# Kernel tuning notes

Measured on AMD Instinct MI355X. Metric: run time of the kernel, lower is better.

Reference implementation:

```python
import jax, jax.numpy as jnp
import numpy as np

B, T, H, LAT, ADIM = 8192, 40, 100, 10, 2
ATT_TEMP = 5.0


def setup_inputs() -> dict:
    key = jax.random.key(0)
    ks = jax.random.split(key, 12)
    return {
        "sampled_att_z": jax.random.normal(ks[0], (B, LAT), jnp.float32),
        "enc_h": jax.random.normal(ks[1], (B, H), jnp.float32),
        # keep IDM params strictly positive / physically plausible to avoid inf
        "idm_params": 1.0 + 2.0 * jax.random.uniform(ks[2], (B, 5), jnp.float32),
        "idm_s": jax.random.uniform(ks[3], (B, T, 8), jnp.float32),
        "sdv_acts": jax.random.normal(ks[4], (B, T, ADIM), jnp.float32),
        "linear_W": jax.random.normal(ks[5], (LAT, H), jnp.float32) / np.float32(np.sqrt(LAT)),
        "linear_b": jnp.zeros((H,), jnp.float32),
        "lstm_Wx": jax.random.normal(ks[6], (H + ADIM, 4 * H), jnp.float32) / np.float32(np.sqrt(H + ADIM)),
        "lstm_Wh": jax.random.normal(ks[7], (H, 4 * H), jnp.float32) / np.float32(np.sqrt(H)),
        "lstm_b": jnp.zeros((4 * H,), jnp.float32),
        "att_W": jax.random.normal(ks[8], (H, 1), jnp.float32) / np.float32(np.sqrt(H)),
        "att_b": jnp.zeros((1,), jnp.float32),
        # precomputed per-step noise, replacing tf.random.normal inside the loop
        "noise_f": jax.random.normal(ks[9], (T, B, 1), jnp.float32),
        "noise_m": jax.random.normal(ks[10], (T, B, 1), jnp.float32),
    }


def reference(sampled_att_z, enc_h, idm_params, idm_s, sdv_acts,
              linear_W, linear_b, lstm_Wx, lstm_Wh, lstm_b, att_W, att_b,
              noise_f, noise_m):
    desired_v = idm_params[:, 0:1]
    desired_tgap = idm_params[:, 1:2]
    min_jamx = idm_params[:, 2:3]
    max_act = idm_params[:, 3:4]
    min_act = idm_params[:, 4:5]

    def idm_driver(vel, dv, dx):  # all [B,1]
        dx = jnp.clip(dx, 0.5, 1000.0)
        desired_gap = min_jamx + jax.nn.relu(
            desired_tgap * vel + vel * dv / (2.0 * jnp.sqrt(max_act * min_act)))
        act = max_act * (1.0 - (vel / desired_v) ** 4 - (desired_gap / dx) ** 2)
        return jnp.clip(act, -3.0, 3.0)

    att_proj = sampled_att_z @ linear_W + linear_b  # [B,H]; also the att_context and init h,c

    s_tm = jnp.swapaxes(idm_s, 0, 1)      # [T,B,8]
    a_tm = jnp.swapaxes(sdv_acts, 0, 1)   # [T,B,ADIM]

    ego_v0 = idm_s[:, 0, 0:1]
    ego_x0 = idm_s[:, 0, 3:4]
    zero_act = jnp.zeros_like(ego_v0)  # step-0 kinematic update is a no-op

    def step(carry, xs):
        ego_v, ego_x, h, c, act = carry
        s, sdv, nf, nm = xs
        ego_v = ego_v + act * 0.1
        ego_x = ego_x + ego_v * 0.1 + 0.5 * act * 0.1 ** 2

        f_v, m_v = s[:, 1:2], s[:, 2:3]
        f_x, m_x = s[:, 4:5], s[:, 5:6]
        f_ex, m_ex = s[:, 6:7], s[:, 7:8]

        ef_act = idm_driver(ego_v, ego_v - f_v, f_x - ego_x)
        ef_act = f_ex * ef_act + (1.0 - f_ex) * nf
        em_act = idm_driver(ego_v, ego_v - m_v, m_x - ego_x)
        em_act = m_ex * em_act + (1.0 - m_ex) * nm

        x_in = jnp.concatenate([att_proj, sdv], axis=-1)  # [B,H+ADIM]
        z = x_in @ lstm_Wx + h @ lstm_Wh + lstm_b          # [B,4H], keras gate order i,f,g,o
        zi, zf, zg, zo = jnp.split(z, 4, axis=-1)
        c = jax.nn.sigmoid(zf) * c + jax.nn.sigmoid(zi) * jnp.tanh(zg)
        h = jax.nn.sigmoid(zo) * jnp.tanh(c)

        att_score = jax.nn.sigmoid(ATT_TEMP * (h @ att_W + att_b))  # [B,1]
        act = (1.0 - att_score) * ef_act + att_score * em_act
        return (ego_v, ego_x, h, c, act), (act, att_score)

    init = (ego_v0, ego_x0, att_proj, att_proj, zero_act)
    _, (acts, atts) = jax.lax.scan(step, init, (s_tm, a_tm, noise_f, noise_m))
    act_seq = jnp.swapaxes(acts, 0, 1)  # [B,T,1]
    att_seq = jnp.swapaxes(atts, 0, 1)  # [B,T,1]
    return act_seq, att_seq
```

## Files before the change

### kernel.cpp

```cpp
#include <hip/hip_runtime.h>
#include <math.h>


#define B_TOT 8192
#define T_STEPS 40
#define NB 16

typedef _Float16 f16;
typedef f16 f16x8 __attribute__((ext_vector_type(8)));
typedef float f32x4 __attribute__((ext_vector_type(4)));

__device__ __forceinline__ float rcpf(float x) { return __builtin_amdgcn_rcpf(x); }
__device__ __forceinline__ float ex2(float x)  { return __builtin_amdgcn_exp2f(x); }
__device__ __forceinline__ float sigf(float x)  { return rcpf(1.f + ex2(-1.44269504f * x)); }


__global__ __launch_bounds__(256) void idm_prep(
    const float* __restrict__ Wx, const float* __restrict__ Wh,
    const float* __restrict__ bvec, const float* __restrict__ attw,
    const float* __restrict__ attB,
    f16* __restrict__ whb, f16* __restrict__ wxb,
    float* __restrict__ bp)
{
  int i = blockIdx.x * 256 + threadIdx.x;
  int k = i >> 9, n = i & 511;
  int g = n >> 7, j128 = n & 127;
  float sc = (g == 2) ? 2.88539008f : 1.44269504f;
  float vh = 0.f, vx = 0.f;
  if (j128 < 100) {
    int col = g * 100 + j128;
    if (k < 100)      { vh = Wh[k * 400 + col] * sc; vx = Wx[k * 400 + col] * sc; }
    else if (k < 102) { vh = Wx[k * 400 + col] * sc; }
  } else if (n == 100 && k < 100) {
    vh = attw[k];
  }
  int idx = (((n >> 4) * 4 + (k >> 5)) * 64 + (((k >> 3) & 3) * 16 + (n & 15))) * 8 + (k & 7);
  whb[idx] = (f16)vh;
  wxb[idx] = (f16)vx;
  if (i < 512) {
    int gg = i >> 7, jj = i & 127;
    float scb = (gg == 2) ? 2.88539008f : 1.44269504f;
    bp[i] = (jj < 100) ? bvec[gg * 100 + jj] * scb
                       : ((i == 100) ? attB[0] : 0.f);
  }
}

#define MM(z, a, g, kf) z = __builtin_amdgcn_mfma_f32_16x16x32_f16(a, wb[g][kf], z, 0, 0, 0)

#define TAIL_STEP(tt) {                                                        \
    int tt_ = (tt);                                                            \
    float inv_dv = pS[0][l], des_tg = pS[1][l], min_jx = pS[2][l];             \
    float max_a = pS[3][l], inv2s = pS[4][l];                                  \
    float2 s01 = *(const float2*)&sS[l][tt_][0];                               \
    float2 s23 = *(const float2*)&sS[l][tt_][2];                               \
    float2 s45 = *(const float2*)&sS[l][tt_][4];                               \
    float nf = nS[0][tt_][l], nm = nS[1][tt_][l];                              \
    float lg = logitS[tt_][l];                                                 \
    ego_v += actT * 0.1f;                                                      \
    ego_x += ego_v * 0.1f + actT * 0.005f;                                     \
    float dxf = fminf(fmaxf(s23.x - ego_x, 0.5f), 1000.f);                     \
    float dgf = min_jx + fmaxf(0.f, des_tg * ego_v + ego_v * (ego_v - s01.x) * inv2s); \
    float rr = ego_v * inv_dv; float rr2 = rr * rr;                            \
    float qf = dgf * rcpf(dxf);                                                \
    float af_ = fminf(fmaxf(max_a * (1.f - rr2 * rr2 - qf * qf), -3.f), 3.f);  \
    float dxm = fminf(fmaxf(s23.y - ego_x, 0.5f), 1000.f);                     \
    float dgm = min_jx + fmaxf(0.f, des_tg * ego_v + ego_v * (ego_v - s01.y) * inv2s); \
    float qm = dgm * rcpf(dxm);                                                \
    float am_ = fminf(fmaxf(max_a * (1.f - rr2 * rr2 - qm * qm), -3.f), 3.f);  \
    float ef2 = s45.x * af_ + (1.f - s45.x) * nf;                              \
    float em2 = s45.y * am_ + (1.f - s45.y) * nm;                              \
    float att = sigf(5.f * lg);                                                \
    actT = (1.f - att) * ef2 + att * em2;                                      \
    accS[0][l][tt_] = actT;                                                    \
    accS[1][l][tt_] = att;                                                     \
  }

__global__ __launch_bounds__(448, 4) void idm_main(
    const float* __restrict__ z_att,
    const float* __restrict__ linear_W,
    const float* __restrict__ linear_b,
    const float* __restrict__ sdv_acts,
    const f16* __restrict__ whb, const f16* __restrict__ wxb,
    const float* __restrict__ bp,
    const float* __restrict__ idm_params,
    const float* __restrict__ idm_s,
    const float* __restrict__ noise_f,
    const float* __restrict__ noise_m,
    float* __restrict__ out)
{
  __shared__ f16   hS[2][16][136];
  __shared__ f16   sdvS[T_STEPS][16][2];
  __shared__ float logitS[T_STEPS][16];
  __shared__ float sS[16][T_STEPS][6];
  __shared__ float nS[2][T_STEPS][16];
  __shared__ float accS[2][16][T_STEPS];
  __shared__ float pS[5][16];

  const int tid = threadIdx.x;
  const int w  = tid >> 6;
  const int l  = tid & 63;
  const int lr = l & 15;
  const int lq = l >> 4;
  const int b0g = blockIdx.x * NB;
  const int jcol = 16 * w + lr;
  const bool tail_lane = (tid < NB);

  for (int idx = tid; idx < 2176; idx += 448) ((unsigned*)hS)[idx] = 0u;
  for (int idx = tid; idx < 1280; idx += 448) {
    float v = sdv_acts[(size_t)b0g * 80 + idx];
    int b = idx / 80, r = idx - b * 80;
    sdvS[r >> 1][b][r & 1] = (f16)v;
  }
  for (int idx = tid; idx < 5120; idx += 448) {
    int f = idx & 7;
    if (f != 0 && f != 3) {
      int b = idx / 320, rem = idx - b * 320, t = rem >> 3;
      sS[b][t][(f < 3) ? f - 1 : f - 2] = idm_s[(size_t)b0g * 320 + idx];
    }
  }
  for (int idx = tid; idx < 1280; idx += 448) {
    int which = idx >= 640 ? 1 : 0;
    int r = idx - which * 640;
    int t = r >> 4, i = r & 15;
    nS[which][t][i] = which ? noise_m[(size_t)t * B_TOT + b0g + i]
                            : noise_f[(size_t)t * B_TOT + b0g + i];
  }
  if (tid < 80) pS[tid % 5][tid / 5] = idm_params[(size_t)b0g * 5 + tid];
  __syncthreads();

  if (tid < 16) {
    pS[0][tid] = rcpf(pS[0][tid]);
    pS[4][tid] = 0.5f / sqrtf(pS[3][tid] * pS[4][tid]);
  }

  if (tid >= 64 && tid < 320) {
    int s2 = tid - 64;
    int b = s2 >> 4, oct = s2 & 15;
    float za[10];
    #pragma unroll
    for (int t2 = 0; t2 < 10; ++t2) za[t2] = z_att[(b0g + b) * 10 + t2];
    #pragma unroll
    for (int jj = 0; jj < 8; ++jj) {
      int j = oct * 8 + jj;
      if (j < 100) {
        float acc = linear_b[j];
        #pragma unroll
        for (int t2 = 0; t2 < 10; ++t2) acc = fmaf(za[t2], linear_W[t2 * 100 + j], acc);
        hS[0][b][j] = (f16)acc;
      }
    }
  }
  if (tid < 32) hS[0][tid >> 1][100 + (tid & 1)] = sdvS[0][tid >> 1][tid & 1];
  __syncthreads();

  f16x8 wb[4][4];
  #pragma unroll
  for (int g = 0; g < 4; ++g) {
    int tile = w + 8 * g;
    #pragma unroll
    for (int kf = 0; kf < 4; ++kf)
      wb[g][kf] = *(const f16x8*)(wxb + ((size_t)(tile * 4 + kf) * 64 + l) * 8);
  }
  f32x4 cx[4];
  #pragma unroll
  for (int g = 0; g < 4; ++g) {
    float bpv = bp[(w + 8 * g) * 16 + lr];
    f32x4 c = {bpv, bpv, bpv, bpv};
    cx[g] = c;
  }
  #pragma unroll
  for (int kf = 0; kf < 4; ++kf) {
    f16x8 a = *(const f16x8*)(&hS[0][lr][kf * 32 + lq * 8]);
    #pragma unroll
    for (int g = 0; g < 4; ++g)
      cx[g] = __builtin_amdgcn_mfma_f32_16x16x32_f16(a, wb[g][kf], cx[g], 0, 0, 0);
  }
  #pragma unroll
  for (int g = 0; g < 4; ++g) {
    int tile = w + 8 * g;
    #pragma unroll
    for (int kf = 0; kf < 4; ++kf)
      wb[g][kf] = *(const f16x8*)(whb + ((size_t)(tile * 4 + kf) * 64 + l) * 8);
  }

  float cst[4];
  #pragma unroll
  for (int r = 0; r < 4; ++r) cst[r] = (float)hS[0][lq * 4 + r][jcol];

  float ego_v = 0.f, ego_x = 0.f, actT = 0.f;
  if (tail_lane) {
    ego_v = idm_s[(size_t)(b0g + l) * 320 + 0];
    ego_x = idm_s[(size_t)(b0g + l) * 320 + 3];
  }

  int p = 0;
  for (int t = 0; t < T_STEPS; ++t) {
    f16x8 a0 = *(const f16x8*)(&hS[p][lr][0  + lq * 8]);
    f16x8 a1 = *(const f16x8*)(&hS[p][lr][32 + lq * 8]);
    f16x8 a2 = *(const f16x8*)(&hS[p][lr][64 + lq * 8]);
    f16x8 a3 = *(const f16x8*)(&hS[p][lr][96 + lq * 8]);
    f32x4 z0 = cx[0], z1 = cx[1], z2 = cx[2], z3 = cx[3];
    MM(z0,a0,0,0); MM(z1,a0,1,0); MM(z2,a0,2,0); MM(z3,a0,3,0);
    MM(z0,a1,0,1); MM(z1,a1,1,1); MM(z2,a1,2,1); MM(z3,a1,3,1);
    MM(z0,a2,0,2); MM(z1,a2,1,2); MM(z2,a2,2,2); MM(z3,a2,3,2);
    MM(z0,a3,0,3); MM(z1,a3,1,3); MM(z2,a3,2,3); MM(z3,a3,3,3);

    if (w == 6 && t > 0 && lr == 4) {
      #pragma unroll
      for (int r = 0; r < 4; ++r) logitS[t - 1][lq * 4 + r] = z0[r];
    }

    #pragma unroll
    for (int r = 0; r < 4; ++r) {
      float e0 = ex2(-z0[r]);
      float e1 = ex2(-z1[r]);
      float e2 = fminf(ex2(z2[r]), 1e30f);
      float e3 = ex2(-z3[r]);
      float sf  = rcpf(1.f + e1);
      float itg = (e2 - 1.f) * rcpf((1.f + e0) * (1.f + e2));
      float cc  = fmaf(sf, cst[r], itg);
      float d   = fminf(ex2(2.88539008f * cc), 1e30f);
      float hh  = (d - 1.f) * rcpf((1.f + e3) * (1.f + d));
      cst[r] = cc;
      if (jcol < 100) hS[p ^ 1][lq * 4 + r][jcol] = (f16)hh;
    }
    if (t + 1 < T_STEPS && tid < 32)
      hS[p ^ 1][tid >> 1][100 + (tid & 1)] = sdvS[t + 1][tid >> 1][tid & 1];
    if (tail_lane && t >= 2) TAIL_STEP(t - 2);
    __syncthreads();
    p ^= 1;
  }

  if (w == 6) {
    float bpv6 = bp[96 + lr];
    f32x4 zL = {bpv6, bpv6, bpv6, bpv6};
    #pragma unroll
    for (int kf = 0; kf < 4; ++kf) {
      f16x8 a = *(const f16x8*)(&hS[p][lr][kf * 32 + lq * 8]);
      zL = __builtin_amdgcn_mfma_f32_16x16x32_f16(a, wb[0][kf], zL, 0, 0, 0);
    }
    if (lr == 4) {
      #pragma unroll
      for (int r = 0; r < 4; ++r) logitS[T_STEPS - 1][lq * 4 + r] = zL[r];
    }
  }
  if (tail_lane) TAIL_STEP(T_STEPS - 2);
  __syncthreads();
  if (tail_lane) TAIL_STEP(T_STEPS - 1);
  __syncthreads();

  if (tid < 160) {
    f32x4 va = ((const f32x4*)&accS[0][0][0])[tid];
    f32x4 vt = ((const f32x4*)&accS[1][0][0])[tid];
    *(f32x4*)(out + (size_t)b0g * T_STEPS + tid * 4) = va;
    *(f32x4*)(out + (size_t)B_TOT * T_STEPS + (size_t)b0g * T_STEPS + tid * 4) = vt;
  }
}

extern "C" void kernel_launch(void* const* d_in, const int* in_sizes, int n_in,
                              void* d_out, int out_size, void* d_ws, size_t ws_size,
                              hipStream_t stream) {
  const float* z_att      = (const float*)d_in[0];
  const float* idm_params = (const float*)d_in[2];
  const float* idm_s      = (const float*)d_in[3];
  const float* sdv_acts   = (const float*)d_in[4];
  const float* linear_W   = (const float*)d_in[5];
  const float* linear_b   = (const float*)d_in[6];
  const float* lstm_Wx    = (const float*)d_in[7];
  const float* lstm_Wh    = (const float*)d_in[8];
  const float* lstm_b     = (const float*)d_in[9];
  const float* att_W      = (const float*)d_in[10];
  const float* att_b      = (const float*)d_in[11];
  const float* noise_f    = (const float*)d_in[12];
  const float* noise_m    = (const float*)d_in[13];
  float* out = (float*)d_out;

  f16*   whb = (f16*)d_ws;
  f16*   wxb = (f16*)((char*)d_ws + 131072);
  float* bp  = (float*)((char*)d_ws + 262144);

  idm_prep<<<256, 256, 0, stream>>>(lstm_Wx, lstm_Wh, lstm_b, att_W, att_b,
                                    whb, wxb, bp);
  idm_main<<<B_TOT / NB, 448, 0, stream>>>(z_att, linear_W, linear_b, sdv_acts,
                                           whb, wxb, bp,
                                           idm_params, idm_s,
                                           noise_f, noise_m, out);
}
```

Baseline: 174.8 us.

## Ping-pong two batch groups per block to overlap MFMA with gate math

Doubles the batch rows per block to 32 and splits the 14 waves into two groups of 16 rows each. The groups alternate each half-step, so one group's MFMA gate matmul runs while the other group does the transcendental LSTM cell update and IDM tail. The aim is to hide the serial dependency between the matmul and the elementwise work within one block. The cost is twice as many block barriers per timestep and half as many blocks, which may cut the natural overlap the hardware already gets from co-resident blocks.

```diff
diff --git a/kernel.cpp b/kernel.cpp
--- a/kernel.cpp
+++ b/kernel.cpp
@@ -4,7 +4,7 @@
 
 #define B_TOT 8192
 #define T_STEPS 40
-#define NB 16
+#define NB 32
 
 typedef _Float16 f16;
 typedef f16 f16x8 __attribute__((ext_vector_type(8)));
@@ -47,15 +47,15 @@
 
 #define MM(z, a, g, kf) z = __builtin_amdgcn_mfma_f32_16x16x32_f16(a, wb[g][kf], z, 0, 0, 0)
 
-#define TAIL_STEP(tt) {                                                        \
-    int tt_ = (tt);                                                            \
-    float inv_dv = pS[0][l], des_tg = pS[1][l], min_jx = pS[2][l];             \
-    float max_a = pS[3][l], inv2s = pS[4][l];                                  \
-    float2 s01 = *(const float2*)&sS[l][tt_][0];                               \
-    float2 s23 = *(const float2*)&sS[l][tt_][2];                               \
-    float2 s45 = *(const float2*)&sS[l][tt_][4];                               \
-    float nf = nS[0][tt_][l], nm = nS[1][tt_][l];                              \
-    float lg = logitS[tt_][l];                                                 \
+#define TAIL_STEP(tt, lb) {                                                    \
+    int tt_ = (tt); int lb_ = (lb);                                            \
+    float inv_dv = pS[0][lb_], des_tg = pS[1][lb_], min_jx = pS[2][lb_];       \
+    float max_a = pS[3][lb_], inv2s = pS[4][lb_];                              \
+    float2 s01 = *(const float2*)&sS[lb_][tt_][0];                             \
+    float2 s23 = *(const float2*)&sS[lb_][tt_][2];                             \
+    float2 s45 = *(const float2*)&sS[lb_][tt_][4];                             \
+    float nf = nS[0][tt_][lb_], nm = nS[1][tt_][lb_];                          \
+    float lg = logitS[tt_][lb_];                                               \
     ego_v += actT * 0.1f;                                                      \
     ego_x += ego_v * 0.1f + actT * 0.005f;                                     \
     float dxf = fminf(fmaxf(s23.x - ego_x, 0.5f), 1000.f);                     \
@@ -71,11 +71,11 @@
     float em2 = s45.y * am_ + (1.f - s45.y) * nm;                              \
     float att = sigf(5.f * lg);                                                \
     actT = (1.f - att) * ef2 + att * em2;                                      \
-    accS[0][l][tt_] = actT;                                                    \
-    accS[1][l][tt_] = att;                                                     \
-  }
-
-__global__ __launch_bounds__(448, 4) void idm_main(
+    accS[0][lb_][tt_] = actT;                                                  \
+    accS[1][lb_][tt_] = att;                                                   \
+  }
+
+__global__ __launch_bounds__(896, 4) void idm_main(
     const float* __restrict__ z_att,
     const float* __restrict__ linear_W,
     const float* __restrict__ linear_b,
@@ -89,56 +89,57 @@
     float* __restrict__ out)
 {
   __shared__ f16   hS[2][16][136];
-  __shared__ f16   sdvS[T_STEPS][16][2];
-  __shared__ float logitS[T_STEPS][16];
-  __shared__ float sS[16][T_STEPS][6];
-  __shared__ float nS[2][T_STEPS][16];
-  __shared__ float accS[2][16][T_STEPS];
-  __shared__ float pS[5][16];
+  __shared__ f16   sdvS[T_STEPS][32][2];
+  __shared__ float logitS[T_STEPS][32];
+  __shared__ float sS[32][T_STEPS][6];
+  __shared__ float nS[2][T_STEPS][32];
+  __shared__ float accS[2][32][T_STEPS];
+  __shared__ float pS[5][32];
 
   const int tid = threadIdx.x;
-  const int w  = tid >> 6;
+  const int w   = tid >> 6;
+  const int grp = (w >= 7) ? 1 : 0;
+  const int wv  = grp ? (w - 7) : w;
   const int l  = tid & 63;
   const int lr = l & 15;
   const int lq = l >> 4;
   const int b0g = blockIdx.x * NB;
-  const int jcol = 16 * w + lr;
-  const bool tail_lane = (tid < NB);
-
-  for (int idx = tid; idx < 2176; idx += 448) ((unsigned*)hS)[idx] = 0u;
-  for (int idx = tid; idx < 1280; idx += 448) {
+  const int jcol = 16 * wv + lr;
+
+  for (int idx = tid; idx < 2176; idx += 896) ((unsigned*)hS)[idx] = 0u;
+  for (int idx = tid; idx < 2560; idx += 896) {
     float v = sdv_acts[(size_t)b0g * 80 + idx];
     int b = idx / 80, r = idx - b * 80;
     sdvS[r >> 1][b][r & 1] = (f16)v;
   }
-  for (int idx = tid; idx < 5120; idx += 448) {
+  for (int idx = tid; idx < 10240; idx += 896) {
     int f = idx & 7;
     if (f != 0 && f != 3) {
       int b = idx / 320, rem = idx - b * 320, t = rem >> 3;
       sS[b][t][(f < 3) ? f - 1 : f - 2] = idm_s[(size_t)b0g * 320 + idx];
     }
   }
-  for (int idx = tid; idx < 1280; idx += 448) {
-    int which = idx >= 640 ? 1 : 0;
-    int r = idx - which * 640;
-    int t = r >> 4, i = r & 15;
+  for (int idx = tid; idx < 2560; idx += 896) {
+    int which = idx >= 1280 ? 1 : 0;
+    int r = idx - which * 1280;
+    int t = r >> 5, i = r & 31;
     nS[which][t][i] = which ? noise_m[(size_t)t * B_TOT + b0g + i]
                             : noise_f[(size_t)t * B_TOT + b0g + i];
   }
-  if (tid < 80) pS[tid % 5][tid / 5] = idm_params[(size_t)b0g * 5 + tid];
-  __syncthreads();
-
-  if (tid < 16) {
+  if (tid < 160) pS[tid % 5][tid / 5] = idm_params[(size_t)b0g * 5 + tid];
+  __syncthreads();
+
+  if (tid < 32) {
     pS[0][tid] = rcpf(pS[0][tid]);
     pS[4][tid] = 0.5f / sqrtf(pS[3][tid] * pS[4][tid]);
   }
 
-  if (tid >= 64 && tid < 320) {
+  if (tid >= 64 && tid < 576) {
     int s2 = tid - 64;
-    int b = s2 >> 4, oct = s2 & 15;
+    int lb = s2 >> 4, oct = s2 & 15;
     float za[10];
     #pragma unroll
-    for (int t2 = 0; t2 < 10; ++t2) za[t2] = z_att[(b0g + b) * 10 + t2];
+    for (int t2 = 0; t2 < 10; ++t2) za[t2] = z_att[(size_t)(b0g + lb) * 10 + t2];
     #pragma unroll
     for (int jj = 0; jj < 8; ++jj) {
       int j = oct * 8 + jj;
@@ -146,17 +147,17 @@
         float acc = linear_b[j];
         #pragma unroll
         for (int t2 = 0; t2 < 10; ++t2) acc = fmaf(za[t2], linear_W[t2 * 100 + j], acc);
-        hS[0][b][j] = (f16)acc;
-      }
-    }
-  }
-  if (tid < 32) hS[0][tid >> 1][100 + (tid & 1)] = sdvS[0][tid >> 1][tid & 1];
+        hS[lb >> 4][lb & 15][j] = (f16)acc;
+      }
+    }
+  }
+  if (tid < 64) hS[tid >> 5][(tid >> 1) & 15][100 + (tid & 1)] = sdvS[0][tid >> 1][tid & 1];
   __syncthreads();
 
   f16x8 wb[4][4];
   #pragma unroll
   for (int g = 0; g < 4; ++g) {
-    int tile = w + 8 * g;
+    int tile = wv + 8 * g;
     #pragma unroll
     for (int kf = 0; kf < 4; ++kf)
       wb[g][kf] = *(const f16x8*)(wxb + ((size_t)(tile * 4 + kf) * 64 + l) * 8);
@@ -164,20 +165,20 @@
   f32x4 cx[4];
   #pragma unroll
   for (int g = 0; g < 4; ++g) {
-    float bpv = bp[(w + 8 * g) * 16 + lr];
+    float bpv = bp[(wv + 8 * g) * 16 + lr];
     f32x4 c = {bpv, bpv, bpv, bpv};
     cx[g] = c;
   }
   #pragma unroll
   for (int kf = 0; kf < 4; ++kf) {
-    f16x8 a = *(const f16x8*)(&hS[0][lr][kf * 32 + lq * 8]);
+    f16x8 a = *(const f16x8*)(&hS[grp][lr][kf * 32 + lq * 8]);
     #pragma unroll
     for (int g = 0; g < 4; ++g)
       cx[g] = __builtin_amdgcn_mfma_f32_16x16x32_f16(a, wb[g][kf], cx[g], 0, 0, 0);
   }
   #pragma unroll
   for (int g = 0; g < 4; ++g) {
-    int tile = w + 8 * g;
+    int tile = wv + 8 * g;
     #pragma unroll
     for (int kf = 0; kf < 4; ++kf)
       wb[g][kf] = *(const f16x8*)(whb + ((size_t)(tile * 4 + kf) * 64 + l) * 8);
@@ -185,31 +186,73 @@
 
   float cst[4];
   #pragma unroll
-  for (int r = 0; r < 4; ++r) cst[r] = (float)hS[0][lq * 4 + r][jcol];
+  for (int r = 0; r < 4; ++r) cst[r] = (float)hS[grp][lq * 4 + r][jcol];
 
   float ego_v = 0.f, ego_x = 0.f, actT = 0.f;
-  if (tail_lane) {
-    ego_v = idm_s[(size_t)(b0g + l) * 320 + 0];
-    ego_x = idm_s[(size_t)(b0g + l) * 320 + 3];
-  }
-
-  int p = 0;
-  for (int t = 0; t < T_STEPS; ++t) {
-    f16x8 a0 = *(const f16x8*)(&hS[p][lr][0  + lq * 8]);
-    f16x8 a1 = *(const f16x8*)(&hS[p][lr][32 + lq * 8]);
-    f16x8 a2 = *(const f16x8*)(&hS[p][lr][64 + lq * 8]);
-    f16x8 a3 = *(const f16x8*)(&hS[p][lr][96 + lq * 8]);
-    f32x4 z0 = cx[0], z1 = cx[1], z2 = cx[2], z3 = cx[3];
-    MM(z0,a0,0,0); MM(z1,a0,1,0); MM(z2,a0,2,0); MM(z3,a0,3,0);
-    MM(z0,a1,0,1); MM(z1,a1,1,1); MM(z2,a1,2,1); MM(z3,a1,3,1);
-    MM(z0,a2,0,2); MM(z1,a2,1,2); MM(z2,a2,2,2); MM(z3,a2,3,2);
-    MM(z0,a3,0,3); MM(z1,a3,1,3); MM(z2,a3,2,3); MM(z3,a3,3,3);
-
-    if (w == 6 && t > 0 && lr == 4) {
+  if (wv == 0 && l < 16) {
+    int b = b0g + grp * 16 + l;
+    ego_v = idm_s[(size_t)b * 320 + 0];
+    ego_x = idm_s[(size_t)b * 320 + 3];
+  }
+
+  f32x4 z0, z1, z2, z3;
+
+  for (int hi = 0; hi < 2 * T_STEPS; ++hi) {
+    int ph = hi & 1, step = hi >> 1;
+    if (ph == grp) {
+      f16x8 a0 = *(const f16x8*)(&hS[grp][lr][0  + lq * 8]);
+      f16x8 a1 = *(const f16x8*)(&hS[grp][lr][32 + lq * 8]);
+      f16x8 a2 = *(const f16x8*)(&hS[grp][lr][64 + lq * 8]);
+      f16x8 a3 = *(const f16x8*)(&hS[grp][lr][96 + lq * 8]);
+      z0 = cx[0]; z1 = cx[1]; z2 = cx[2]; z3 = cx[3];
+      MM(z0,a0,0,0); MM(z1,a0,1,0); MM(z2,a0,2,0); MM(z3,a0,3,0);
+      MM(z0,a1,0,1); MM(z1,a1,1,1); MM(z2,a1,2,1); MM(z3,a1,3,1);
+      MM(z0,a2,0,2); MM(z1,a2,1,2); MM(z2,a2,2,2); MM(z3,a2,3,2);
+      MM(z0,a3,0,3); MM(z1,a3,1,3); MM(z2,a3,2,3); MM(z3,a3,3,3);
+      if (wv == 6 && step > 0 && lr == 4) {
+        #pragma unroll
+        for (int r = 0; r < 4; ++r) logitS[step - 1][grp * 16 + lq * 4 + r] = z0[r];
+      }
+    } else {
+      int gstep = step - grp;
+      if (gstep >= 0) {
+        #pragma unroll
+        for (int r = 0; r < 4; ++r) {
+          float e0 = ex2(-z0[r]);
+          float e1 = ex2(-z1[r]);
+          float e2 = fminf(ex2(z2[r]), 1e30f);
+          float e3 = ex2(-z3[r]);
+          float sf  = rcpf(1.f + e1);
+          float itg = (e2 - 1.f) * rcpf((1.f + e0) * (1.f + e2));
+          float cc  = fmaf(sf, cst[r], itg);
+          float d   = fminf(ex2(2.88539008f * cc), 1e30f);
+          float hh  = (d - 1.f) * rcpf((1.f + e3) * (1.f + d));
+          cst[r] = cc;
+          if (jcol < 100) hS[grp][lq * 4 + r][jcol] = (f16)hh;
+        }
+        if (wv == 1 && l < 32 && gstep + 1 < T_STEPS)
+          hS[grp][l >> 1][100 + (l & 1)] = sdvS[gstep + 1][grp * 16 + (l >> 1)][l & 1];
+        if (wv == 0 && l < 16 && gstep >= 1) TAIL_STEP(gstep - 1, grp * 16 + l);
+      }
+    }
+    __syncthreads();
+  }
+
+  if (grp == 0) {
+    if (wv == 6) {
+      float bpv6 = bp[96 + lr];
+      f32x4 zL = {bpv6, bpv6, bpv6, bpv6};
       #pragma unroll
-      for (int r = 0; r < 4; ++r) logitS[t - 1][lq * 4 + r] = z0[r];
-    }
-
+      for (int kf = 0; kf < 4; ++kf) {
+        f16x8 a = *(const f16x8*)(&hS[0][lr][kf * 32 + lq * 8]);
+        zL = __builtin_amdgcn_mfma_f32_16x16x32_f16(a, wb[0][kf], zL, 0, 0, 0);
+      }
+      if (lr == 4) {
+        #pragma unroll
+        for (int r = 0; r < 4; ++r) logitS[T_STEPS - 1][lq * 4 + r] = zL[r];
+      }
+    }
+  } else {
     #pragma unroll
     for (int r = 0; r < 4; ++r) {
       float e0 = ex2(-z0[r]);
@@ -222,34 +265,30 @@
       float d   = fminf(ex2(2.88539008f * cc), 1e30f);
       float hh  = (d - 1.f) * rcpf((1.f + e3) * (1.f + d));
       cst[r] = cc;
-      if (jcol < 100) hS[p ^ 1][lq * 4 + r][jcol] = (f16)hh;
-    }
-    if (t + 1 < T_STEPS && tid < 32)
-      hS[p ^ 1][tid >> 1][100 + (tid & 1)] = sdvS[t + 1][tid >> 1][tid & 1];
-    if (tail_lane && t >= 2) TAIL_STEP(t - 2);
-    __syncthreads();
-    p ^= 1;
-  }
-
-  if (w == 6) {
+      if (jcol < 100) hS[1][lq * 4 + r][jcol] = (f16)hh;
+    }
+    if (wv == 0 && l < 16) TAIL_STEP(T_STEPS - 2, 16 + l);
+  }
+  __syncthreads();
+  if (grp == 1 && wv == 6) {
     float bpv6 = bp[96 + lr];
     f32x4 zL = {bpv6, bpv6, bpv6, bpv6};
     #pragma unroll
     for (int kf = 0; kf < 4; ++kf) {
-      f16x8 a = *(const f16x8*)(&hS[p][lr][kf * 32 + lq * 8]);
+      f16x8 a = *(const f16x8*)(&hS[1][lr][kf * 32 + lq * 8]);
       zL = __builtin_amdgcn_mfma_f32_16x16x32_f16(a, wb[0][kf], zL, 0, 0, 0);
     }
     if (lr == 4) {
       #pragma unroll
-      for (int r = 0; r < 4; ++r) logitS[T_STEPS - 1][lq * 4 + r] = zL[r];
-    }
-  }
-  if (tail_lane) TAIL_STEP(T_STEPS - 2);
-  __syncthreads();
-  if (tail_lane) TAIL_STEP(T_STEPS - 1);
-  __syncthreads();
-
-  if (tid < 160) {
+      for (int r = 0; r < 4; ++r) logitS[T_STEPS - 1][16 + lq * 4 + r] = zL[r];
+    }
+  }
+  if (grp == 0 && wv == 0 && l < 16) TAIL_STEP(T_STEPS - 1, l);
+  __syncthreads();
+  if (grp == 1 && wv == 0 && l < 16) TAIL_STEP(T_STEPS - 1, 16 + l);
+  __syncthreads();
+
+  if (tid < 320) {
     f32x4 va = ((const f32x4*)&accS[0][0][0])[tid];
     f32x4 vt = ((const f32x4*)&accS[1][0][0])[tid];
     *(f32x4*)(out + (size_t)b0g * T_STEPS + tid * 4) = va;
@@ -281,7 +320,7 @@
 
   idm_prep<<<256, 256, 0, stream>>>(lstm_Wx, lstm_Wh, lstm_b, att_W, att_b,
                                     whb, wxb, bp);
-  idm_main<<<B_TOT / NB, 448, 0, stream>>>(z_att, linear_W, linear_b, sdv_acts,
+  idm_main<<<B_TOT / NB, 896, 0, stream>>>(z_att, linear_W, linear_b, sdv_acts,
                                            whb, wxb, bp,
                                            idm_params, idm_s,
                                            noise_f, noise_m, out);
```

After: 185.1 us. 1.06x slower.
